# Performance work log

Hardware: AMD Instinct MI355X
Metric: run time of the kernel (lower is better)

Reference implementation:

```python
import jax, jax.numpy as jnp
import numpy as np

N_CHEM = 100000
N_PROT = 20000
D = 128           # hidden_channels, also input feature dim (lazy SAGEConv)
E = 600000        # edges chem->protein (reverse relation uses flipped index)
EL = 200000       # label edges for decoder
L = 3             # SAGEConv layers


def setup_inputs() -> dict:
    key = jax.random.key(0)
    ks = jax.random.split(key, 11)
    inp = {
        'x_chem':    jax.random.normal(ks[0], (N_CHEM, D), jnp.float32),
        'x_protein': jax.random.normal(ks[1], (N_PROT, D), jnp.float32),
        # Wl/bl/Wr stacked over [layer, relation]; relation 0 = chem->protein (dst protein),
        # relation 1 = protein->chem (dst chem). PyG SAGEConv: lin_l has bias, lin_r does not.
        'Wl': jax.random.normal(ks[2], (L, 2, D, D), jnp.float32) * 0.05,
        'bl': jax.random.normal(ks[3], (L, 2, D), jnp.float32) * 0.05,
        'Wr': jax.random.normal(ks[4], (L, 2, D, D), jnp.float32) * 0.05,
        'Wd': jax.random.normal(ks[5], (1, 2 * D), jnp.float32) * 0.05,
        'bd': jax.random.normal(ks[6], (1,), jnp.float32) * 0.05,
        'src_idx': jax.random.randint(ks[7], (E,), 0, N_CHEM, jnp.int64),
        'dst_idx': jax.random.randint(ks[8], (E,), 0, N_PROT, jnp.int64),
        'row': jax.random.randint(ks[9], (EL,), 0, N_CHEM, jnp.int64),
        'col': jax.random.randint(ks[10], (EL,), 0, N_PROT, jnp.int64),
    }
    return inp


def _sage(x_src, x_dst, s_idx, d_idx, Wl, bl, Wr, n_dst):
    # PyG SAGEConv (aggr='mean'): lin_l(mean_j x_src[j]) + lin_r(x_dst)
    msg = x_src[s_idx]                                   # [E, D] gather
    agg = jax.ops.segment_sum(msg, d_idx, num_segments=n_dst)
    deg = jax.ops.segment_sum(jnp.ones((s_idx.shape[0],), x_src.dtype), d_idx,
                              num_segments=n_dst)
    mean = agg / jnp.clip(deg, 1.0)[:, None]
    return mean @ Wl.T + bl + x_dst @ Wr.T


def reference(x_chem, x_protein, Wl, bl, Wr, Wd, bd, src_idx, dst_idx, row, col):
    h_c, h_p = x_chem, x_protein
    for l in range(L):
        new_p = _sage(h_c, h_p, src_idx, dst_idx, Wl[l, 0], bl[l, 0], Wr[l, 0], N_PROT)
        new_c = _sage(h_p, h_c, dst_idx, src_idx, Wl[l, 1], bl[l, 1], Wr[l, 1], N_CHEM)
        h_c, h_p = jax.nn.relu(new_c), jax.nn.relu(new_p)
    # EdgeDecoder: gather + concat + linear -> flat scores
    x = jnp.concatenate([h_c[row], h_p[col]], axis=-1)   # [EL, 2D]
    z = (x @ Wd.T + bd).reshape(-1)                      # [EL]
    return (z, x)
```

## Files before the change

### kernel.cpp

```cpp
#include <hip/hip_runtime.h>

#define D128 128

typedef __attribute__((ext_vector_type(8))) short bf16x8;
typedef __attribute__((ext_vector_type(4))) float f32x4;
typedef unsigned short u16;

__device__ __forceinline__ u16 f2b(float f) {
  union { float f; unsigned int u; } x; x.f = f;
  unsigned int r = x.u + 0x7fffu + ((x.u >> 16) & 1u);
  return (u16)(r >> 16);
}

#define GLD16(gp, lp) __builtin_amdgcn_global_load_lds( \
    (const __attribute__((address_space(1))) void*)(gp), \
    (__attribute__((address_space(3))) void*)(lp), 16, 0, 0)


__global__ __launch_bounds__(256) void cvt_all_k(const float* __restrict__ xc, const float* __restrict__ xp,
                                                 const float* __restrict__ Wl, const float* __restrict__ Wr,
                                                 u16* __restrict__ xcb, u16* __restrict__ xpb,
                                                 u16* __restrict__ Wcat, int* __restrict__ zbase,
                                                 int n4c, int n4p, int wq, int zq) {
  int TOT = n4c + n4p + wq + zq;
  for (int i = blockIdx.x * 256 + threadIdx.x; i < TOT; i += gridDim.x * 256) {
    if (i < n4c + n4p) {
      const float* src = (i < n4c) ? xc : xp;
      u16* dst = (i < n4c) ? xcb : xpb;
      int q = (i < n4c) ? i : (i - n4c);
      float4 f = ((const float4*)src)[q];
      uint2 u;
      u.x = (unsigned)f2b(f.x) | ((unsigned)f2b(f.y) << 16);
      u.y = (unsigned)f2b(f.z) | ((unsigned)f2b(f.w) << 16);
      ((uint2*)dst)[q] = u;
    } else if (i < n4c + n4p + wq) {
      int t = (i - n4c - n4p) * 4;
      int slice = t >> 15;
      int j = (t >> 8) & 127;
      int k = t & 255;
      const float* sw = (k < 128) ? (Wl + (size_t)slice * 16384 + j * 128 + k)
                                  : (Wr + (size_t)slice * 16384 + j * 128 + (k - 128));
      float4 f = *(const float4*)sw;
      uint2 u;
      u.x = (unsigned)f2b(f.x) | ((unsigned)f2b(f.y) << 16);
      u.y = (unsigned)f2b(f.z) | ((unsigned)f2b(f.w) << 16);
      *(uint2*)&Wcat[t] = u;
    } else {
      int z = i - n4c - n4p - wq;
      int4 zv; zv.x = 0; zv.y = 0; zv.z = 0; zv.w = 0;
      ((int4*)zbase)[z] = zv;
    }
  }
}


__global__ __launch_bounds__(256) void degree_k(const int* __restrict__ src, const int* __restrict__ dst,
                                                int* deg, int NP, int E) {
  int e = blockIdx.x * 256 + threadIdx.x;
  if (e >= E) return;
  atomicAdd(&deg[dst[e]], 1);
  atomicAdd(&deg[NP + src[e]], 1);
}

__global__ __launch_bounds__(256) void scan1_k(const int* __restrict__ in, int* __restrict__ out,
                                               int* __restrict__ bsum, int n) {
  __shared__ int sh[256];
  int tid = threadIdx.x;
  int base = blockIdx.x * 2048 + tid * 8;
  int v[8]; int s = 0;
#pragma unroll
  for (int u = 0; u < 8; ++u) { int i = base + u; v[u] = (i < n) ? in[i] : 0; s += v[u]; }
  sh[tid] = s; __syncthreads();
#pragma unroll
  for (int o = 1; o < 256; o <<= 1) {
    int t = (tid >= o) ? sh[tid - o] : 0;
    __syncthreads();
    sh[tid] += t;
    __syncthreads();
  }
  int run = sh[tid] - s;
  if (tid == 255) bsum[blockIdx.x] = sh[255];
#pragma unroll
  for (int u = 0; u < 8; ++u) { int i = base + u; if (i < n) out[i] = run; run += v[u]; }
}

__global__ void scan_small_k(int* b, int n) {
  __shared__ int sh[64];
  int tid = threadIdx.x;
  int v = (tid < n) ? b[tid] : 0;
  sh[tid] = v; __syncthreads();
  for (int o = 1; o < 64; o <<= 1) {
    int t = (tid >= o) ? sh[tid - o] : 0;
    __syncthreads();
    sh[tid] += t;
    __syncthreads();
  }
  if (tid < n) b[tid] = sh[tid] - v;
}

__global__ __launch_bounds__(256) void scan_add_k(int* out, const int* __restrict__ bsum, int n) {
  int b = blockIdx.x;
  if (b == 0) return;
  int add = bsum[b];
  int base = b * 2048;
  for (int i = threadIdx.x; i < 2048; i += 256) { int idx = base + i; if (idx < n) out[idx] += add; }
}

__global__ __launch_bounds__(256) void fill_k(const int* __restrict__ src, const int* __restrict__ dst,
                                              const int* __restrict__ off, int* cur, int* adj,
                                              int NP, int E) {
  int e = blockIdx.x * 256 + threadIdx.x;
  if (e >= E) return;
  int s = src[e], d = dst[e];
  int pp = atomicAdd(&cur[d], 1); adj[off[d] + pp] = s;
  int pc = atomicAdd(&cur[NP + s], 1); adj[off[NP + s] + pc] = d;
}


__global__ __launch_bounds__(256) void agg_all_k(const u16* __restrict__ hc, const u16* __restrict__ hp,
                                                 u16* __restrict__ meanC, u16* __restrict__ meanP,
                                                 const int* __restrict__ adj, const int* __restrict__ off,
                                                 const int* __restrict__ deg, int NP, int NT) {
  int v = blockIdx.x * 4 + (threadIdx.x >> 6);
  if (v >= NT) return;
  int lane = threadIdx.x & 63;
  bool isP = v < NP;
  const u16* __restrict__ src = isP ? hc : hp;
  u16* outm = isP ? (meanP + (size_t)v * D128) : (meanC + (size_t)(v - NP) * D128);
  int s = off[v], cnt = deg[v];
  int l2 = lane * 2;
  float a0x = 0.f, a0y = 0.f, a1x = 0.f, a1y = 0.f;
  float a2x = 0.f, a2y = 0.f, a3x = 0.f, a3y = 0.f;
  int n = 0;
  while (n < cnt) {
    int batch = cnt - n; if (batch > 64) batch = 64;
    int idx = (lane < batch) ? adj[s + n + lane] : 0;
    int j = 0;
    for (; j + 4 <= batch; j += 4) {
      int i0 = __shfl(idx, j);
      int i1 = __shfl(idx, j + 1);
      int i2 = __shfl(idx, j + 2);
      int i3 = __shfl(idx, j + 3);
      unsigned u0 = *(const unsigned*)&src[(size_t)i0 * D128 + l2];
      unsigned u1 = *(const unsigned*)&src[(size_t)i1 * D128 + l2];
      unsigned u2 = *(const unsigned*)&src[(size_t)i2 * D128 + l2];
      unsigned u3 = *(const unsigned*)&src[(size_t)i3 * D128 + l2];
      a0x += __uint_as_float(u0 << 16); a0y += __uint_as_float(u0 & 0xffff0000u);
      a1x += __uint_as_float(u1 << 16); a1y += __uint_as_float(u1 & 0xffff0000u);
      a2x += __uint_as_float(u2 << 16); a2y += __uint_as_float(u2 & 0xffff0000u);
      a3x += __uint_as_float(u3 << 16); a3y += __uint_as_float(u3 & 0xffff0000u);
    }
    for (; j < batch; ++j) {
      int i0 = __shfl(idx, j);
      unsigned u0 = *(const unsigned*)&src[(size_t)i0 * D128 + l2];
      a0x += __uint_as_float(u0 << 16); a0y += __uint_as_float(u0 & 0xffff0000u);
    }
    n += batch;
  }
  float sx = (a0x + a1x) + (a2x + a3x);
  float sy = (a0y + a1y) + (a2y + a3y);
  float inv = (cnt > 0) ? 1.f / (float)cnt : 0.f;
  unsigned pk = (unsigned)f2b(sx * inv) | ((unsigned)f2b(sy * inv) << 16);
  *(unsigned*)&outm[l2] = pk;
}


__global__ __launch_bounds__(256) void gemm_both_k(u16* __restrict__ np_, u16* __restrict__ nc,
                                                   const u16* __restrict__ hp, const u16* __restrict__ hc,
                                                   const u16* __restrict__ Wcat_l, const float* __restrict__ bl_l,
                                                   int NP, int NC, int tilesP) {
  __shared__ u16 As[128 * 64];
  __shared__ u16 Bs[128 * 64];
  const int b = blockIdx.x;
  const bool isP = b < tilesP;
  const int rbase = (isP ? b : b - tilesP) * 128;
  u16* __restrict__ io_mean = isP ? np_ : nc;
  const u16* __restrict__ hold = isP ? hp : hc;
  const u16* __restrict__ Wcat = Wcat_l + (isP ? 0 : 128 * 256);
  const float* __restrict__ bias = bl_l + (isP ? 0 : 128);
  const int N = isP ? NP : NC;

  const int tid = threadIdx.x;
  const int w = tid >> 6, lane = tid & 63;
  const int wr = w >> 1, wc = w & 1;
  const int l15 = lane & 15, chi = lane >> 4;

  f32x4 acc[4][4];
#pragma unroll
  for (int m = 0; m < 4; ++m)
#pragma unroll
    for (int n = 0; n < 4; ++n) acc[m][n] = (f32x4){0.f, 0.f, 0.f, 0.f};

  for (int ks = 0; ks < 4; ++ks) {
    const int k0 = ks * 64;
    const u16* Xsrc = (k0 < 128) ? io_mean : hold;
    const int kb = k0 & 127;
    if (ks) __syncthreads();
#pragma unroll
    for (int q = 0; q < 4; ++q) {
      const int ibase = w * 256 + q * 64;
      const int i = ibase + lane;
      const int r = i >> 3;
      const int cg = (i & 7) ^ (r & 7);
      int rr = rbase + r; if (rr >= N) rr = N - 1;
      const u16* gp = Xsrc + (size_t)rr * D128 + kb + cg * 8;
      GLD16(gp, (char*)As + ibase * 16);
      const u16* gw = Wcat + (size_t)r * 256 + k0 + cg * 8;
      GLD16(gw, (char*)Bs + ibase * 16);
    }
    __syncthreads();
#pragma unroll
    for (int kk = 0; kk < 2; ++kk) {
      bf16x8 a[4], bf[4];
      const int c = kk * 4 + chi;
#pragma unroll
      for (int m = 0; m < 4; ++m) {
        const int r = wr * 64 + m * 16 + l15;
        a[m] = *(const bf16x8*)((const char*)As + (r * 8 + (c ^ (r & 7))) * 16);
      }
#pragma unroll
      for (int n = 0; n < 4; ++n) {
        const int j = wc * 64 + n * 16 + l15;
        bf[n] = *(const bf16x8*)((const char*)Bs + (j * 8 + (c ^ (j & 7))) * 16);
      }
#pragma unroll
      for (int m = 0; m < 4; ++m)
#pragma unroll
        for (int n = 0; n < 4; ++n)
          acc[m][n] = __builtin_amdgcn_mfma_f32_16x16x32_bf16(a[m], bf[n], acc[m][n], 0, 0, 0);
    }
  }

#pragma unroll
  for (int n = 0; n < 4; ++n) {
    const int col = wc * 64 + n * 16 + l15;
    const float bv = bias[col];
#pragma unroll
    for (int m = 0; m < 4; ++m) {
      const int rb2 = rbase + wr * 64 + m * 16 + chi * 4;
#pragma unroll
      for (int q = 0; q < 4; ++q) {
        const int row = rb2 + q;
        if (row < N) {
          float vv = acc[m][n][q] + bv;
          vv = vv > 0.f ? vv : 0.f;
          io_mean[(size_t)row * D128 + col] = f2b(vv);
        }
      }
    }
  }
}


__global__ __launch_bounds__(256) void decoder_b_k(const u16* __restrict__ hc, const u16* __restrict__ hp,
                                                   const int* __restrict__ row, const int* __restrict__ col,
                                                   const float* __restrict__ Wd, const float* __restrict__ bd,
                                                   float* __restrict__ out, int EL) {
  int e = blockIdx.x * 4 + (threadIdx.x >> 6);
  if (e >= EL) return;
  int lane = threadIdx.x & 63;
  int l2 = lane * 2;
  int r = row[e], c = col[e];
  unsigned ua = *(const unsigned*)&hc[(size_t)r * D128 + l2];
  unsigned ub = *(const unsigned*)&hp[(size_t)c * D128 + l2];
  float ax = __uint_as_float(ua << 16), ay = __uint_as_float(ua & 0xffff0000u);
  float bx = __uint_as_float(ub << 16), by = __uint_as_float(ub & 0xffff0000u);
  float2 w0 = *(const float2*)&Wd[l2];
  float2 w1 = *(const float2*)&Wd[128 + l2];
  float p = ax * w0.x + ay * w0.y + bx * w1.x + by * w1.y;
#pragma unroll
  for (int m = 1; m < 64; m <<= 1) p += __shfl_xor(p, m, 64);
  float* xo = out + EL + (size_t)e * 256;
  float2 A; A.x = ax; A.y = ay;
  float2 B; B.x = bx; B.y = by;
  *(float2*)&xo[l2] = A;
  *(float2*)&xo[128 + l2] = B;
  if (lane == 0) out[e] = p + bd[0];
}


extern "C" void kernel_launch(void* const* d_in, const int* in_sizes, int n_in,
                              void* d_out, int out_size, void* d_ws, size_t ws_size,
                              hipStream_t stream) {
  const float* x_chem = (const float*)d_in[0];
  const float* x_prot = (const float*)d_in[1];
  const float* Wl = (const float*)d_in[2];
  const float* bl = (const float*)d_in[3];
  const float* Wr = (const float*)d_in[4];
  const float* Wd = (const float*)d_in[5];
  const float* bd = (const float*)d_in[6];
  const int* src = (const int*)d_in[7];
  const int* dst = (const int*)d_in[8];
  const int* row = (const int*)d_in[9];
  const int* col = (const int*)d_in[10];

  int NC = in_sizes[0] / D128;
  int NP = in_sizes[1] / D128;
  int E  = in_sizes[7];
  int EL = in_sizes[9];
  float* out = (float*)d_out;
  int NT = NP + NC;

  char* w = (char*)d_ws;
  size_t szC = (size_t)NC * D128 * 2;
  size_t szP = (size_t)NP * D128 * 2;
  u16* xc_bf = (u16*)w; w += szC;
  u16* xp_bf = (u16*)w; w += szP;
  u16* bufC0 = (u16*)w; w += szC;
  u16* bufC1 = (u16*)w; w += szC;
  u16* bufP0 = (u16*)w; w += szP;
  u16* bufP1 = (u16*)w; w += szP;
  u16* Wcat  = (u16*)w; w += (size_t)6 * 128 * 256 * 2;
  int* deg = (int*)w; w += (size_t)NT * 4;
  int* cur = (int*)w; w += (size_t)NT * 4;
  int* off = (int*)w; w += (size_t)NT * 4;
  int* bs  = (int*)w; w += 64 * 4;
  int* adj = (int*)w; w += (size_t)2 * E * 4;
  if ((size_t)(w - (char*)d_ws) > ws_size) return;

  int n4c = NC * D128 / 4, n4p = NP * D128 / 4;
  int wq = 6 * 128 * 256 / 4;
  int zq = 2 * NT / 4;
  cvt_all_k<<<2048, 256, 0, stream>>>(x_chem, x_prot, Wl, Wr, xc_bf, xp_bf, Wcat, deg,
                                      n4c, n4p, wq, zq);

  int gE = (E + 255) / 256;
  degree_k<<<gE, 256, 0, stream>>>(src, dst, deg, NP, E);
  int nb = (NT + 2047) / 2048;
  scan1_k<<<nb, 256, 0, stream>>>(deg, off, bs, NT);
  scan_small_k<<<1, 64, 0, stream>>>(bs, nb);
  scan_add_k<<<nb, 256, 0, stream>>>(off, bs, NT);
  fill_k<<<gE, 256, 0, stream>>>(src, dst, off, cur, adj, NP, E);

  int tilesP = (NP + 127) / 128;
  int tilesC = (NC + 127) / 128;
  const u16* hc = xc_bf;
  const u16* hp = xp_bf;
  for (int l = 0; l < 3; ++l) {
    u16* nc  = (l & 1) ? bufC1 : bufC0;
    u16* np_ = (l & 1) ? bufP1 : bufP0;
    const u16* Wc_l = Wcat + (size_t)(l * 2) * 128 * 256;
    const float* bl_l = bl + (size_t)(l * 2) * D128;
    agg_all_k<<<(NT + 3) / 4, 256, 0, stream>>>(hc, hp, nc, np_, adj, off, deg, NP, NT);
    gemm_both_k<<<tilesP + tilesC, 256, 0, stream>>>(np_, nc, hp, hc, Wc_l, bl_l, NP, NC, tilesP);
    hc = nc; hp = np_;
  }

  decoder_b_k<<<(EL + 3) / 4, 256, 0, stream>>>(hc, hp, row, col, Wd, bd, out, EL);
}
```

Measured before the change: 486.8 us.

## Fuse all stages into one persistent kernel with grid-wide barriers

Replaces the sequence of separate kernel launches (convert, degree, scan, fill, per-layer aggregate and GEMM, decoder) with a single persistent mega-kernel sized to occupancy, separated by atomic-counter grid barriers. It also merges chem and protein features into one unified node buffer, widens the aggregation gather to 16-byte loads with 16 lanes per node, and reworks the scan to use chunk prefixes. The aim is to remove launch overhead and inter-kernel gaps. In exchange, the spin-wait barriers cost time, and the persistent grid may lose load balance and occupancy, especially in the GEMM phase, which is capped at 3 blocks per CU.

```diff
diff --git a/kernel.cpp b/kernel.cpp
--- a/kernel.cpp
+++ b/kernel.cpp
@@ -5,277 +5,291 @@
 typedef __attribute__((ext_vector_type(8))) short bf16x8;
 typedef __attribute__((ext_vector_type(4))) float f32x4;
 typedef unsigned short u16;
+typedef unsigned int u32;
 
 __device__ __forceinline__ u16 f2b(float f) {
-  union { float f; unsigned int u; } x; x.f = f;
-  unsigned int r = x.u + 0x7fffu + ((x.u >> 16) & 1u);
+  union { float f; u32 u; } x; x.f = f;
+  u32 r = x.u + 0x7fffu + ((x.u >> 16) & 1u);
   return (u16)(r >> 16);
+}
+__device__ __forceinline__ float b2f(short s) {
+  union { u32 u; float f; } x; x.u = ((u32)(unsigned short)s) << 16; return x.f;
 }
 
 #define GLD16(gp, lp) __builtin_amdgcn_global_load_lds( \
     (const __attribute__((address_space(1))) void*)(gp), \
     (__attribute__((address_space(3))) void*)(lp), 16, 0, 0)
 
-
-__global__ __launch_bounds__(256) void cvt_all_k(const float* __restrict__ xc, const float* __restrict__ xp,
-                                                 const float* __restrict__ Wl, const float* __restrict__ Wr,
-                                                 u16* __restrict__ xcb, u16* __restrict__ xpb,
-                                                 u16* __restrict__ Wcat, int* __restrict__ zbase,
-                                                 int n4c, int n4p, int wq, int zq) {
-  int TOT = n4c + n4p + wq + zq;
-  for (int i = blockIdx.x * 256 + threadIdx.x; i < TOT; i += gridDim.x * 256) {
-    if (i < n4c + n4p) {
-      const float* src = (i < n4c) ? xc : xp;
-      u16* dst = (i < n4c) ? xcb : xpb;
-      int q = (i < n4c) ? i : (i - n4c);
-      float4 f = ((const float4*)src)[q];
-      uint2 u;
-      u.x = (unsigned)f2b(f.x) | ((unsigned)f2b(f.y) << 16);
-      u.y = (unsigned)f2b(f.z) | ((unsigned)f2b(f.w) << 16);
-      ((uint2*)dst)[q] = u;
-    } else if (i < n4c + n4p + wq) {
-      int t = (i - n4c - n4p) * 4;
-      int slice = t >> 15;
-      int j = (t >> 8) & 127;
-      int k = t & 255;
-      const float* sw = (k < 128) ? (Wl + (size_t)slice * 16384 + j * 128 + k)
-                                  : (Wr + (size_t)slice * 16384 + j * 128 + (k - 128));
-      float4 f = *(const float4*)sw;
-      uint2 u;
-      u.x = (unsigned)f2b(f.x) | ((unsigned)f2b(f.y) << 16);
-      u.y = (unsigned)f2b(f.z) | ((unsigned)f2b(f.w) << 16);
-      *(uint2*)&Wcat[t] = u;
-    } else {
-      int z = i - n4c - n4p - wq;
-      int4 zv; zv.x = 0; zv.y = 0; zv.z = 0; zv.w = 0;
-      ((int4*)zbase)[z] = zv;
-    }
-  }
-}
-
-
-__global__ __launch_bounds__(256) void degree_k(const int* __restrict__ src, const int* __restrict__ dst,
-                                                int* deg, int NP, int E) {
-  int e = blockIdx.x * 256 + threadIdx.x;
-  if (e >= E) return;
-  atomicAdd(&deg[dst[e]], 1);
-  atomicAdd(&deg[NP + src[e]], 1);
-}
-
-__global__ __launch_bounds__(256) void scan1_k(const int* __restrict__ in, int* __restrict__ out,
-                                               int* __restrict__ bsum, int n) {
-  __shared__ int sh[256];
-  int tid = threadIdx.x;
-  int base = blockIdx.x * 2048 + tid * 8;
-  int v[8]; int s = 0;
-#pragma unroll
-  for (int u = 0; u < 8; ++u) { int i = base + u; v[u] = (i < n) ? in[i] : 0; s += v[u]; }
-  sh[tid] = s; __syncthreads();
-#pragma unroll
-  for (int o = 1; o < 256; o <<= 1) {
-    int t = (tid >= o) ? sh[tid - o] : 0;
-    __syncthreads();
-    sh[tid] += t;
-    __syncthreads();
-  }
-  int run = sh[tid] - s;
-  if (tid == 255) bsum[blockIdx.x] = sh[255];
-#pragma unroll
-  for (int u = 0; u < 8; ++u) { int i = base + u; if (i < n) out[i] = run; run += v[u]; }
-}
-
-__global__ void scan_small_k(int* b, int n) {
-  __shared__ int sh[64];
-  int tid = threadIdx.x;
-  int v = (tid < n) ? b[tid] : 0;
-  sh[tid] = v; __syncthreads();
-  for (int o = 1; o < 64; o <<= 1) {
-    int t = (tid >= o) ? sh[tid - o] : 0;
-    __syncthreads();
-    sh[tid] += t;
-    __syncthreads();
-  }
-  if (tid < n) b[tid] = sh[tid] - v;
-}
-
-__global__ __launch_bounds__(256) void scan_add_k(int* out, const int* __restrict__ bsum, int n) {
-  int b = blockIdx.x;
-  if (b == 0) return;
-  int add = bsum[b];
-  int base = b * 2048;
-  for (int i = threadIdx.x; i < 2048; i += 256) { int idx = base + i; if (idx < n) out[idx] += add; }
-}
-
-__global__ __launch_bounds__(256) void fill_k(const int* __restrict__ src, const int* __restrict__ dst,
-                                              const int* __restrict__ off, int* cur, int* adj,
-                                              int NP, int E) {
-  int e = blockIdx.x * 256 + threadIdx.x;
-  if (e >= E) return;
-  int s = src[e], d = dst[e];
-  int pp = atomicAdd(&cur[d], 1); adj[off[d] + pp] = s;
-  int pc = atomicAdd(&cur[NP + s], 1); adj[off[NP + s] + pc] = d;
-}
-
-
-__global__ __launch_bounds__(256) void agg_all_k(const u16* __restrict__ hc, const u16* __restrict__ hp,
-                                                 u16* __restrict__ meanC, u16* __restrict__ meanP,
-                                                 const int* __restrict__ adj, const int* __restrict__ off,
-                                                 const int* __restrict__ deg, int NP, int NT) {
-  int v = blockIdx.x * 4 + (threadIdx.x >> 6);
-  if (v >= NT) return;
-  int lane = threadIdx.x & 63;
-  bool isP = v < NP;
-  const u16* __restrict__ src = isP ? hc : hp;
-  u16* outm = isP ? (meanP + (size_t)v * D128) : (meanC + (size_t)(v - NP) * D128);
-  int s = off[v], cnt = deg[v];
-  int l2 = lane * 2;
-  float a0x = 0.f, a0y = 0.f, a1x = 0.f, a1y = 0.f;
-  float a2x = 0.f, a2y = 0.f, a3x = 0.f, a3y = 0.f;
-  int n = 0;
-  while (n < cnt) {
-    int batch = cnt - n; if (batch > 64) batch = 64;
-    int idx = (lane < batch) ? adj[s + n + lane] : 0;
-    int j = 0;
-    for (; j + 4 <= batch; j += 4) {
-      int i0 = __shfl(idx, j);
-      int i1 = __shfl(idx, j + 1);
-      int i2 = __shfl(idx, j + 2);
-      int i3 = __shfl(idx, j + 3);
-      unsigned u0 = *(const unsigned*)&src[(size_t)i0 * D128 + l2];
-      unsigned u1 = *(const unsigned*)&src[(size_t)i1 * D128 + l2];
-      unsigned u2 = *(const unsigned*)&src[(size_t)i2 * D128 + l2];
-      unsigned u3 = *(const unsigned*)&src[(size_t)i3 * D128 + l2];
-      a0x += __uint_as_float(u0 << 16); a0y += __uint_as_float(u0 & 0xffff0000u);
-      a1x += __uint_as_float(u1 << 16); a1y += __uint_as_float(u1 & 0xffff0000u);
-      a2x += __uint_as_float(u2 << 16); a2y += __uint_as_float(u2 & 0xffff0000u);
-      a3x += __uint_as_float(u3 << 16); a3y += __uint_as_float(u3 & 0xffff0000u);
-    }
-    for (; j < batch; ++j) {
-      int i0 = __shfl(idx, j);
-      unsigned u0 = *(const unsigned*)&src[(size_t)i0 * D128 + l2];
-      a0x += __uint_as_float(u0 << 16); a0y += __uint_as_float(u0 & 0xffff0000u);
-    }
-    n += batch;
-  }
-  float sx = (a0x + a1x) + (a2x + a3x);
-  float sy = (a0y + a1y) + (a2y + a3y);
-  float inv = (cnt > 0) ? 1.f / (float)cnt : 0.f;
-  unsigned pk = (unsigned)f2b(sx * inv) | ((unsigned)f2b(sy * inv) << 16);
-  *(unsigned*)&outm[l2] = pk;
-}
-
-
-__global__ __launch_bounds__(256) void gemm_both_k(u16* __restrict__ np_, u16* __restrict__ nc,
-                                                   const u16* __restrict__ hp, const u16* __restrict__ hc,
-                                                   const u16* __restrict__ Wcat_l, const float* __restrict__ bl_l,
-                                                   int NP, int NC, int tilesP) {
+__device__ __forceinline__ void gbar(int* c, int nb) {
+  __syncthreads();
+  if (threadIdx.x == 0) {
+    __threadfence();
+    __hip_atomic_fetch_add(c, 1, __ATOMIC_RELEASE, __HIP_MEMORY_SCOPE_AGENT);
+    while (__hip_atomic_load(c, __ATOMIC_ACQUIRE, __HIP_MEMORY_SCOPE_AGENT) < nb)
+      __builtin_amdgcn_s_sleep(2);
+  }
+  __syncthreads();
+  __threadfence();
+}
+
+__global__ __launch_bounds__(256, 3) void mega_k(
+    const float* __restrict__ xc, const float* __restrict__ xp,
+    const float* __restrict__ Wl, const float* __restrict__ blp,
+    const float* __restrict__ Wr, const float* __restrict__ Wd,
+    const float* __restrict__ bd,
+    const int* __restrict__ src, const int* __restrict__ dst,
+    const int* __restrict__ rowi, const int* __restrict__ coli,
+    u16* __restrict__ B0, u16* __restrict__ B1, u16* __restrict__ B2,
+    u16* __restrict__ Wcat,
+    int* __restrict__ deg, int* __restrict__ cur, int* __restrict__ offp,
+    int* __restrict__ csum, int* __restrict__ cpref, int* __restrict__ adj,
+    int* cnts, float* __restrict__ out,
+    int NP, int NC, int E, int EL, int nchunk) {
   __shared__ u16 As[128 * 64];
   __shared__ u16 Bs[128 * 64];
-  const int b = blockIdx.x;
-  const bool isP = b < tilesP;
-  const int rbase = (isP ? b : b - tilesP) * 128;
-  u16* __restrict__ io_mean = isP ? np_ : nc;
-  const u16* __restrict__ hold = isP ? hp : hc;
-  const u16* __restrict__ Wcat = Wcat_l + (isP ? 0 : 128 * 256);
-  const float* __restrict__ bias = bl_l + (isP ? 0 : 128);
-  const int N = isP ? NP : NC;
-
   const int tid = threadIdx.x;
-  const int w = tid >> 6, lane = tid & 63;
-  const int wr = w >> 1, wc = w & 1;
-  const int l15 = lane & 15, chi = lane >> 4;
-
-  f32x4 acc[4][4];
-#pragma unroll
-  for (int m = 0; m < 4; ++m)
-#pragma unroll
-    for (int n = 0; n < 4; ++n) acc[m][n] = (f32x4){0.f, 0.f, 0.f, 0.f};
-
-  for (int ks = 0; ks < 4; ++ks) {
-    const int k0 = ks * 64;
-    const u16* Xsrc = (k0 < 128) ? io_mean : hold;
-    const int kb = k0 & 127;
-    if (ks) __syncthreads();
-#pragma unroll
-    for (int q = 0; q < 4; ++q) {
-      const int ibase = w * 256 + q * 64;
-      const int i = ibase + lane;
-      const int r = i >> 3;
-      const int cg = (i & 7) ^ (r & 7);
-      int rr = rbase + r; if (rr >= N) rr = N - 1;
-      const u16* gp = Xsrc + (size_t)rr * D128 + kb + cg * 8;
-      GLD16(gp, (char*)As + ibase * 16);
-      const u16* gw = Wcat + (size_t)r * 256 + k0 + cg * 8;
-      GLD16(gw, (char*)Bs + ibase * 16);
-    }
-    __syncthreads();
-#pragma unroll
-    for (int kk = 0; kk < 2; ++kk) {
-      bf16x8 a[4], bf[4];
-      const int c = kk * 4 + chi;
-#pragma unroll
-      for (int m = 0; m < 4; ++m) {
-        const int r = wr * 64 + m * 16 + l15;
-        a[m] = *(const bf16x8*)((const char*)As + (r * 8 + (c ^ (r & 7))) * 16);
+  const int NT = NP + NC;
+  const int gtid = blockIdx.x * 256 + tid;
+  const int gs = gridDim.x * 256;
+  const int nb = gridDim.x;
+  const int lane = tid & 63;
+  const int wid = blockIdx.x * 4 + (tid >> 6);
+  const int nw = gridDim.x * 4;
+
+  {
+    const int nqx = NT * 32;
+    const int TOT = nqx + 49152 + (2 * NT) / 4;
+    for (int i = gtid; i < TOT; i += gs) {
+      if (i < nqx) {
+        const int r = i >> 5, c4 = (i & 31) << 2;
+        const float* sp = (r < NP) ? &xp[(size_t)r * D128 + c4]
+                                   : &xc[(size_t)(r - NP) * D128 + c4];
+        float4 f = *(const float4*)sp;
+        uint2 u;
+        u.x = (u32)f2b(f.x) | ((u32)f2b(f.y) << 16);
+        u.y = (u32)f2b(f.z) | ((u32)f2b(f.w) << 16);
+        *(uint2*)&B0[(size_t)i * 4] = u;
+      } else if (i < nqx + 49152) {
+        const int t = (i - nqx) * 4;
+        const int slice = t >> 15, j = (t >> 8) & 127, k = t & 255;
+        const float* sw = (k < 128) ? &Wl[(size_t)slice * 16384 + j * 128 + k]
+                                    : &Wr[(size_t)slice * 16384 + j * 128 + (k - 128)];
+        float4 f = *(const float4*)sw;
+        uint2 u;
+        u.x = (u32)f2b(f.x) | ((u32)f2b(f.y) << 16);
+        u.y = (u32)f2b(f.z) | ((u32)f2b(f.w) << 16);
+        *(uint2*)&Wcat[t] = u;
+      } else {
+        const int z = i - nqx - 49152;
+        int4 zv; zv.x = 0; zv.y = 0; zv.z = 0; zv.w = 0;
+        ((int4*)deg)[z] = zv;
       }
-#pragma unroll
-      for (int n = 0; n < 4; ++n) {
-        const int j = wc * 64 + n * 16 + l15;
-        bf[n] = *(const bf16x8*)((const char*)Bs + (j * 8 + (c ^ (j & 7))) * 16);
+    }
+  }
+  gbar(cnts + 0, nb);
+
+  for (int e = gtid; e < E; e += gs) {
+    atomicAdd(&deg[dst[e]], 1);
+    atomicAdd(&deg[NP + src[e]], 1);
+  }
+  gbar(cnts + 1, nb);
+
+  {
+    int* sh = (int*)As;
+    for (int c = blockIdx.x; c < nchunk; c += gridDim.x) {
+      const int base = c * 2048 + tid * 8;
+      int v[8]; int s = 0;
+#pragma unroll
+      for (int u = 0; u < 8; ++u) { int i = base + u; v[u] = (i < NT) ? deg[i] : 0; s += v[u]; }
+      sh[tid] = s; __syncthreads();
+#pragma unroll
+      for (int o = 1; o < 256; o <<= 1) {
+        int t = (tid >= o) ? sh[tid - o] : 0;
+        __syncthreads();
+        sh[tid] += t;
+        __syncthreads();
       }
-#pragma unroll
-      for (int m = 0; m < 4; ++m)
-#pragma unroll
-        for (int n = 0; n < 4; ++n)
-          acc[m][n] = __builtin_amdgcn_mfma_f32_16x16x32_bf16(a[m], bf[n], acc[m][n], 0, 0, 0);
-    }
-  }
-
-#pragma unroll
-  for (int n = 0; n < 4; ++n) {
-    const int col = wc * 64 + n * 16 + l15;
-    const float bv = bias[col];
-#pragma unroll
-    for (int m = 0; m < 4; ++m) {
-      const int rb2 = rbase + wr * 64 + m * 16 + chi * 4;
-#pragma unroll
-      for (int q = 0; q < 4; ++q) {
-        const int row = rb2 + q;
-        if (row < N) {
-          float vv = acc[m][n][q] + bv;
-          vv = vv > 0.f ? vv : 0.f;
-          io_mean[(size_t)row * D128 + col] = f2b(vv);
+      int run = sh[tid] - s;
+      if (tid == 255) csum[c] = sh[255];
+#pragma unroll
+      for (int u = 0; u < 8; ++u) { int i = base + u; if (i < NT) offp[i] = run; run += v[u]; }
+      __syncthreads();
+    }
+  }
+  gbar(cnts + 2, nb);
+
+  if (blockIdx.x == 0 && tid < 64) {
+    int v = (tid < nchunk) ? csum[tid] : 0;
+    int x = v;
+#pragma unroll
+    for (int o = 1; o < 64; o <<= 1) {
+      int t = __shfl_up(x, o, 64);
+      if (lane >= o) x += t;
+    }
+    cpref[tid] = x - v;
+  }
+  gbar(cnts + 3, nb);
+
+  for (int e = gtid; e < E; e += gs) {
+    const int s = src[e], d = dst[e];
+    const int cn = NP + s;
+    int pp = atomicAdd(&cur[d], 1);
+    adj[offp[d] + cpref[d >> 11] + pp] = cn;
+    int pc = atomicAdd(&cur[cn], 1);
+    adj[offp[cn] + cpref[cn >> 11] + pc] = d;
+  }
+  gbar(cnts + 4, nb);
+
+  const int tilesP = (NP + 127) >> 7;
+  const int tilesC = (NC + 127) >> 7;
+  for (int l = 0; l < 3; ++l) {
+    const u16* hcur; u16* hnext;
+    if (l == 0)      { hcur = B0; hnext = B1; }
+    else if (l == 1) { hcur = B1; hnext = B2; }
+    else             { hcur = B2; hnext = B1; }
+
+    {
+      const int g = lane >> 4, l16 = lane & 15;
+      for (int n0 = wid * 4; n0 < NT; n0 += nw * 4) {
+        const int v = n0 + g;
+        int s = 0, cnt = 0;
+        if (v < NT) { s = offp[v] + cpref[v >> 11]; cnt = deg[v]; }
+        float ac[8] = {0.f, 0.f, 0.f, 0.f, 0.f, 0.f, 0.f, 0.f};
+        for (int n = 0; n < cnt; n += 16) {
+          int batch = cnt - n; if (batch > 16) batch = 16;
+          int idx = (l16 < batch) ? adj[s + n + l16] : 0;
+          int j = 0;
+          for (; j + 4 <= batch; j += 4) {
+            const int i0 = __shfl(idx, j, 16);
+            const int i1 = __shfl(idx, j + 1, 16);
+            const int i2 = __shfl(idx, j + 2, 16);
+            const int i3 = __shfl(idx, j + 3, 16);
+            bf16x8 r0 = *(const bf16x8*)&hcur[(size_t)i0 * D128 + l16 * 8];
+            bf16x8 r1 = *(const bf16x8*)&hcur[(size_t)i1 * D128 + l16 * 8];
+            bf16x8 r2 = *(const bf16x8*)&hcur[(size_t)i2 * D128 + l16 * 8];
+            bf16x8 r3 = *(const bf16x8*)&hcur[(size_t)i3 * D128 + l16 * 8];
+#pragma unroll
+            for (int k = 0; k < 8; ++k)
+              ac[k] += (b2f(r0[k]) + b2f(r1[k])) + (b2f(r2[k]) + b2f(r3[k]));
+          }
+          for (; j < batch; ++j) {
+            const int i0 = __shfl(idx, j, 16);
+            bf16x8 r0 = *(const bf16x8*)&hcur[(size_t)i0 * D128 + l16 * 8];
+#pragma unroll
+            for (int k = 0; k < 8; ++k) ac[k] += b2f(r0[k]);
+          }
+        }
+        if (v < NT) {
+          const float inv = (cnt > 0) ? 1.f / (float)cnt : 0.f;
+          uint4 pk;
+          pk.x = (u32)f2b(ac[0] * inv) | ((u32)f2b(ac[1] * inv) << 16);
+          pk.y = (u32)f2b(ac[2] * inv) | ((u32)f2b(ac[3] * inv) << 16);
+          pk.z = (u32)f2b(ac[4] * inv) | ((u32)f2b(ac[5] * inv) << 16);
+          pk.w = (u32)f2b(ac[6] * inv) | ((u32)f2b(ac[7] * inv) << 16);
+          *(uint4*)&hnext[(size_t)v * D128 + l16 * 8] = pk;
         }
       }
     }
-  }
-}
-
-
-__global__ __launch_bounds__(256) void decoder_b_k(const u16* __restrict__ hc, const u16* __restrict__ hp,
-                                                   const int* __restrict__ row, const int* __restrict__ col,
-                                                   const float* __restrict__ Wd, const float* __restrict__ bd,
-                                                   float* __restrict__ out, int EL) {
-  int e = blockIdx.x * 4 + (threadIdx.x >> 6);
-  if (e >= EL) return;
-  int lane = threadIdx.x & 63;
-  int l2 = lane * 2;
-  int r = row[e], c = col[e];
-  unsigned ua = *(const unsigned*)&hc[(size_t)r * D128 + l2];
-  unsigned ub = *(const unsigned*)&hp[(size_t)c * D128 + l2];
-  float ax = __uint_as_float(ua << 16), ay = __uint_as_float(ua & 0xffff0000u);
-  float bx = __uint_as_float(ub << 16), by = __uint_as_float(ub & 0xffff0000u);
-  float2 w0 = *(const float2*)&Wd[l2];
-  float2 w1 = *(const float2*)&Wd[128 + l2];
-  float p = ax * w0.x + ay * w0.y + bx * w1.x + by * w1.y;
-#pragma unroll
-  for (int m = 1; m < 64; m <<= 1) p += __shfl_xor(p, m, 64);
-  float* xo = out + EL + (size_t)e * 256;
-  float2 A; A.x = ax; A.y = ay;
-  float2 B; B.x = bx; B.y = by;
-  *(float2*)&xo[l2] = A;
-  *(float2*)&xo[128 + l2] = B;
-  if (lane == 0) out[e] = p + bd[0];
+    gbar(cnts + 5 + l * 2, nb);
+
+    {
+      const int w = tid >> 6;
+      const int wr = w >> 1, wc = w & 1;
+      const int l15 = lane & 15, chi = lane >> 4;
+      for (int t = blockIdx.x; t < tilesP + tilesC; t += gridDim.x) {
+        const bool isP = t < tilesP;
+        const int rbase = isP ? t * 128 : NP + (t - tilesP) * 128;
+        const int hi = isP ? NP : NT;
+        const u16* W = Wcat + (size_t)l * 65536 + (isP ? 0 : 32768);
+        const float* bias = blp + (size_t)l * 256 + (isP ? 0 : 128);
+
+        f32x4 acc[4][4];
+#pragma unroll
+        for (int m = 0; m < 4; ++m)
+#pragma unroll
+          for (int n = 0; n < 4; ++n) acc[m][n] = (f32x4){0.f, 0.f, 0.f, 0.f};
+
+        for (int ks = 0; ks < 4; ++ks) {
+          const int k0 = ks * 64;
+          const u16* Xsrc = (k0 < 128) ? hnext : hcur;
+          const int kb = k0 & 127;
+          __syncthreads();
+#pragma unroll
+          for (int q = 0; q < 4; ++q) {
+            const int ibase = w * 256 + q * 64;
+            const int i = ibase + lane;
+            const int r = i >> 3;
+            const int cg = (i & 7) ^ (r & 7);
+            int rr = rbase + r; if (rr >= hi) rr = hi - 1;
+            GLD16(Xsrc + (size_t)rr * D128 + kb + cg * 8, (char*)As + ibase * 16);
+            GLD16(W + (size_t)r * 256 + k0 + cg * 8, (char*)Bs + ibase * 16);
+          }
+          __syncthreads();
+#pragma unroll
+          for (int kk = 0; kk < 2; ++kk) {
+            bf16x8 a[4], bfr[4];
+            const int c = kk * 4 + chi;
+#pragma unroll
+            for (int m = 0; m < 4; ++m) {
+              const int r = wr * 64 + m * 16 + l15;
+              a[m] = *(const bf16x8*)((const char*)As + (r * 8 + (c ^ (r & 7))) * 16);
+            }
+#pragma unroll
+            for (int n = 0; n < 4; ++n) {
+              const int j = wc * 64 + n * 16 + l15;
+              bfr[n] = *(const bf16x8*)((const char*)Bs + (j * 8 + (c ^ (j & 7))) * 16);
+            }
+#pragma unroll
+            for (int m = 0; m < 4; ++m)
+#pragma unroll
+              for (int n = 0; n < 4; ++n)
+                acc[m][n] = __builtin_amdgcn_mfma_f32_16x16x32_bf16(a[m], bfr[n], acc[m][n], 0, 0, 0);
+          }
+        }
+#pragma unroll
+        for (int n = 0; n < 4; ++n) {
+          const int col = wc * 64 + n * 16 + l15;
+          const float bv = bias[col];
+#pragma unroll
+          for (int m = 0; m < 4; ++m) {
+            const int rb2 = rbase + wr * 64 + m * 16 + chi * 4;
+#pragma unroll
+            for (int q = 0; q < 4; ++q) {
+              const int row = rb2 + q;
+              if (row < hi) {
+                float vv = acc[m][n][q] + bv;
+                vv = vv > 0.f ? vv : 0.f;
+                hnext[(size_t)row * D128 + col] = f2b(vv);
+              }
+            }
+          }
+        }
+      }
+    }
+    gbar(cnts + 6 + l * 2, nb);
+  }
+
+  {
+    const u16* hf = B1;
+    for (int e = wid; e < EL; e += nw) {
+      const int r = rowi[e], c = coli[e];
+      const unsigned ua = *(const unsigned*)&hf[((size_t)(NP + r)) * D128 + lane * 2];
+      const unsigned ub = *(const unsigned*)&hf[((size_t)c) * D128 + lane * 2];
+      const float ax = __uint_as_float(ua << 16), ay = __uint_as_float(ua & 0xffff0000u);
+      const float bx = __uint_as_float(ub << 16), by = __uint_as_float(ub & 0xffff0000u);
+      const float2 w0 = *(const float2*)&Wd[lane * 2];
+      const float2 w1 = *(const float2*)&Wd[128 + lane * 2];
+      float p = ax * w0.x + ay * w0.y + bx * w1.x + by * w1.y;
+#pragma unroll
+      for (int m = 1; m < 64; m <<= 1) p += __shfl_xor(p, m, 64);
+      float* xo = out + EL + (size_t)e * 256;
+      float2 A; A.x = ax; A.y = ay;
+      float2 B; B.x = bx; B.y = by;
+      *(float2*)&xo[lane * 2] = A;
+      *(float2*)&xo[128 + lane * 2] = B;
+      if (lane == 0) out[e] = p + bd[0];
+    }
+  }
 }
 
 
@@ -298,53 +312,40 @@
   int NP = in_sizes[1] / D128;
   int E  = in_sizes[7];
   int EL = in_sizes[9];
+  int NT = NP + NC;
+  int nchunk = (NT + 2047) / 2048;
   float* out = (float*)d_out;
-  int NT = NP + NC;
 
   char* w = (char*)d_ws;
-  size_t szC = (size_t)NC * D128 * 2;
-  size_t szP = (size_t)NP * D128 * 2;
-  u16* xc_bf = (u16*)w; w += szC;
-  u16* xp_bf = (u16*)w; w += szP;
-  u16* bufC0 = (u16*)w; w += szC;
-  u16* bufC1 = (u16*)w; w += szC;
-  u16* bufP0 = (u16*)w; w += szP;
-  u16* bufP1 = (u16*)w; w += szP;
-  u16* Wcat  = (u16*)w; w += (size_t)6 * 128 * 256 * 2;
-  int* deg = (int*)w; w += (size_t)NT * 4;
-  int* cur = (int*)w; w += (size_t)NT * 4;
-  int* off = (int*)w; w += (size_t)NT * 4;
-  int* bs  = (int*)w; w += 64 * 4;
-  int* adj = (int*)w; w += (size_t)2 * E * 4;
+  size_t szT = (size_t)NT * D128 * 2;
+  u16* B0 = (u16*)w; w += szT;
+  u16* B1 = (u16*)w; w += szT;
+  u16* B2 = (u16*)w; w += szT;
+  u16* Wcat = (u16*)w; w += (size_t)6 * 128 * 256 * 2;
+  int* deg  = (int*)w; w += (size_t)NT * 4;
+  int* cur  = (int*)w; w += (size_t)NT * 4;
+  int* offp = (int*)w; w += (size_t)NT * 4;
+  int* csum = (int*)w; w += 64 * 4;
+  int* cpref= (int*)w; w += 64 * 4;
+  int* cnts = (int*)w; w += 64 * 4;
+  int* adj  = (int*)w; w += (size_t)2 * E * 4;
   if ((size_t)(w - (char*)d_ws) > ws_size) return;
 
-  int n4c = NC * D128 / 4, n4p = NP * D128 / 4;
-  int wq = 6 * 128 * 256 / 4;
-  int zq = 2 * NT / 4;
-  cvt_all_k<<<2048, 256, 0, stream>>>(x_chem, x_prot, Wl, Wr, xc_bf, xp_bf, Wcat, deg,
-                                      n4c, n4p, wq, zq);
-
-  int gE = (E + 255) / 256;
-  degree_k<<<gE, 256, 0, stream>>>(src, dst, deg, NP, E);
-  int nb = (NT + 2047) / 2048;
-  scan1_k<<<nb, 256, 0, stream>>>(deg, off, bs, NT);
-  scan_small_k<<<1, 64, 0, stream>>>(bs, nb);
-  scan_add_k<<<nb, 256, 0, stream>>>(off, bs, NT);
-  fill_k<<<gE, 256, 0, stream>>>(src, dst, off, cur, adj, NP, E);
-
-  int tilesP = (NP + 127) / 128;
-  int tilesC = (NC + 127) / 128;
-  const u16* hc = xc_bf;
-  const u16* hp = xp_bf;
-  for (int l = 0; l < 3; ++l) {
-    u16* nc  = (l & 1) ? bufC1 : bufC0;
-    u16* np_ = (l & 1) ? bufP1 : bufP0;
-    const u16* Wc_l = Wcat + (size_t)(l * 2) * 128 * 256;
-    const float* bl_l = bl + (size_t)(l * 2) * D128;
-    agg_all_k<<<(NT + 3) / 4, 256, 0, stream>>>(hc, hp, nc, np_, adj, off, deg, NP, NT);
-    gemm_both_k<<<tilesP + tilesC, 256, 0, stream>>>(np_, nc, hp, hc, Wc_l, bl_l, NP, NC, tilesP);
-    hc = nc; hp = np_;
-  }
-
-  decoder_b_k<<<(EL + 3) / 4, 256, 0, stream>>>(hc, hp, row, col, Wd, bd, out, EL);
-}
+  hipMemsetAsync(cnts, 0, 64 * 4, stream);
+
+  int occ = 0;
+  if (hipOccupancyMaxActiveBlocksPerMultiprocessor(&occ, mega_k, 256, 0) != hipSuccess || occ < 1)
+    occ = 1;
+  int dev = 0;
+  hipGetDevice(&dev);
+  int ncu = 0;
+  if (hipDeviceGetAttribute(&ncu, hipDeviceAttributeMultiprocessorCount, dev) != hipSuccess || ncu < 1)
+    ncu = 256;
+  long long grid = (long long)occ * (long long)ncu;
+  if (grid > 2048) grid = 2048;
+
+  mega_k<<<(int)grid, 256, 0, stream>>>(x_chem, x_prot, Wl, bl, Wr, Wd, bd,
+                                        src, dst, row, col,
+                                        B0, B1, B2, Wcat, deg, cur, offp, csum, cpref, adj,
+                                        cnts, out, NP, NC, E, EL, nchunk);
+}
```

Measured after the change: 1.399 ms. +187.5%, slower.
